# Kernel optimization log

Measured on AMD Instinct MI355X. Metric: run time of the kernel, lower is better.

## Reference

```python
import jax, jax.numpy as jnp
import numpy as np

BETA_MIN = 0.01
BETA_MAX = 0.995
EPS = 1e-6


def setup_inputs() -> dict:
    key = jax.random.key(0)
    k1, k2, k3, k4 = jax.random.split(key, 4)
    B, T, D = 16, 4096, 128
    return {
        "q": jax.random.normal(k1, (B, T, D), dtype=jnp.float32),
        "k": jax.random.normal(k2, (B, T, D), dtype=jnp.float32),
        "v": jax.random.normal(k3, (B, T, D), dtype=jnp.float32),
        "beta": jax.random.uniform(k4, (B, T, 1), dtype=jnp.float32),
        "mask": jnp.ones((B, T, 1), dtype=jnp.float32),
        "base_beta_1": jnp.asarray(2.0, dtype=jnp.float32),
        "base_beta_2": jnp.asarray(3.0, dtype=jnp.float32),
    }


def _delta_scan(q, k, v, beta, mask, base_beta_1, base_beta_2):
    B, T, D = q.shape
    phi_q = jax.nn.elu(q) + 1.0  # positive feature map
    phi_k = jax.nn.elu(k) + 1.0
    b1_base = jnp.clip(jax.nn.sigmoid(base_beta_1), BETA_MIN, BETA_MAX)
    b2_base = jnp.clip(jax.nn.sigmoid(base_beta_2), BETA_MIN, BETA_MAX)

    # time-major for scan: [T, B, ...]
    xs = (
        jnp.swapaxes(phi_q, 0, 1),
        jnp.swapaxes(phi_k, 0, 1),
        jnp.swapaxes(v, 0, 1),
        jnp.swapaxes(beta, 0, 1),
        jnp.swapaxes(mask, 0, 1),
    )

    H1 = jnp.zeros((B, D, D), dtype=q.dtype)
    H2 = jnp.zeros((B, D, D), dtype=q.dtype)
    Z1 = jnp.zeros((B, D), dtype=q.dtype)
    Z2 = jnp.zeros((B, D), dtype=q.dtype)

    def step(carry, x):
        H1, H2, Z1, Z2 = carry
        q_t, k_t, v_t, b_in_t, m_t = x  # q_t:[B,D], b_in_t/m_t:[B,1]
        b_in_t = jnp.clip(b_in_t, BETA_MIN, BETA_MAX)
        b1_t = jnp.clip(b1_base * b_in_t, BETA_MIN, BETA_MAX)  # [B,1]
        b2_t = jnp.clip(b2_base * b_in_t, BETA_MIN, BETA_MAX)
        kv = jnp.einsum('bd,be->bde', k_t, v_t) * m_t[:, :, None]  # masked outer product
        H1 = H1 * b1_t[:, :, None] + kv
        H2 = H2 * b2_t[:, :, None] + kv
        Z1 = Z1 * b1_t + k_t * m_t
        Z2 = Z2 * b2_t + k_t * m_t
        num = jnp.einsum('bd,bde->be', q_t, H1 + H2)
        den = jnp.maximum(jnp.sum(q_t * (Z1 + Z2), axis=-1, keepdims=True), EPS)
        o_t = num / den * m_t
        return (H1, H2, Z1, Z2), o_t

    _, outs = jax.lax.scan(step, (H1, H2, Z1, Z2), xs)
    return jnp.swapaxes(outs, 0, 1)  # [B, T, D]


def reference(q, k, v, beta, mask, base_beta_1, base_beta_2):
    return _delta_scan(q, k, v, beta, mask, base_beta_1, base_beta_2)
```

## Files before the change

### kernel.cpp

```cpp
#include <hip/hip_runtime.h>

#define B_ 16
#define T_ 4096
#define D_ 128
#define L_ 128
#define NC_ 32
#define CH_ (B_*NC_)
#define LDP 136

typedef __attribute__((ext_vector_type(8))) short bf16x8;
typedef __attribute__((ext_vector_type(4))) float f32x4;

__device__ __forceinline__ float clampf(float x, float lo, float hi) {
    return fminf(fmaxf(x, lo), hi);
}
__device__ __forceinline__ float phi_f(float x) {
    return x > 0.f ? x + 1.f : __expf(x);
}
__device__ __forceinline__ unsigned short bf16r(float f) {
    unsigned u = __builtin_bit_cast(unsigned, f);
    u += 0x7FFFu + ((u >> 16) & 1u);
    return (unsigned short)(u >> 16);
}
__device__ __forceinline__ float fbf(unsigned short h) {
    unsigned u = ((unsigned)h) << 16; return __builtin_bit_cast(float, u);
}
__device__ __forceinline__ unsigned pack2bf(float a, float b) {
    return (unsigned)bf16r(a) | ((unsigned)bf16r(b) << 16);
}
__device__ __forceinline__ uint4 pack8(const float* f) {
    uint4 r;
    r.x = pack2bf(f[0], f[1]); r.y = pack2bf(f[2], f[3]);
    r.z = pack2bf(f[4], f[5]); r.w = pack2bf(f[6], f[7]);
    return r;
}
__device__ __forceinline__ f32x4 zero4() { f32x4 z; z[0]=0.f; z[1]=0.f; z[2]=0.f; z[3]=0.f; return z; }

__device__ __forceinline__ int aidx(int row, int k0) {
    return (((row >> 4) * 4 + (k0 >> 5)) * 64 + ((k0 >> 3) & 3) * 16 + (row & 15)) * 8;
}

__global__ __launch_bounds__(256) void kS(
        const float* __restrict__ kk, const float* __restrict__ vv,
        const float* __restrict__ mask,
        const float* __restrict__ beta,
        const float* __restrict__ bb1, const float* __restrict__ bb2,
        unsigned short* __restrict__ phiKT, unsigned short* __restrict__ VtT,
        float* __restrict__ lg1, float* __restrict__ lg2, float* __restrict__ wexp) {
    int g = blockIdx.x;
    int ch = g >> 2, q = g & 3;
    int b = ch / NC_, c = ch % NC_;
    int tbase = b * T_ + c * L_;
    int tid = threadIdx.x;
    size_t cb = (size_t)ch * 16384;
    __shared__ float tot1s[2], tot2s[2];

    float cx1 = 0.f, cx2 = 0.f;
    int clane = tid & 63, cw = tid >> 6;
    if (q == 0 && tid < 128) {
        float b1b = clampf(1.f / (1.f + __expf(-bb1[0])), 0.01f, 0.995f);
        float b2b = clampf(1.f / (1.f + __expf(-bb2[0])), 0.01f, 0.995f);
        float be = clampf(beta[tbase + tid], 0.01f, 0.995f);
        cx1 = __logf(clampf(b1b * be, 0.01f, 0.995f));
        cx2 = __logf(clampf(b2b * be, 0.01f, 0.995f));
#pragma unroll
        for (int off = 1; off < 64; off <<= 1) {
            float y1 = __shfl_up(cx1, off);
            float y2 = __shfl_up(cx2, off);
            if (clane >= off) { cx1 += y1; cx2 += y2; }
        }
        if (clane == 63) { tot1s[cw] = cx1; tot2s[cw] = cx2; }
    }
    __syncthreads();
    if (q == 0 && tid < 128) {
        if (cw == 1) { cx1 += tot1s[0]; cx2 += tot2s[0]; }
        float tot1 = tot1s[0] + tot1s[1];
        float tot2 = tot2s[0] + tot2s[1];
        lg1[tbase + tid] = cx1;
        lg2[tbase + tid] = cx2;
        wexp[(size_t)ch * 128 + tid]                     = __expf(tot1 - cx1);
        wexp[(size_t)CH_ * 128 + (size_t)ch * 128 + tid] = __expf(tot2 - cx2);
    }

#pragma unroll
    for (int p = 0; p < 2; ++p) {
        int i = p * 256 + tid;
        int s = q * 32 + (i >> 4), d0 = (i & 15) * 8;
        const float* kp = &kk[(size_t)(tbase + s) * D_ + d0];
        float4 x0 = *(const float4*)kp, x1 = *(const float4*)(kp + 4);
        float m = mask[tbase + s];
        float pq[8] = {phi_f(x0.x)*m, phi_f(x0.y)*m, phi_f(x0.z)*m, phi_f(x0.w)*m,
                       phi_f(x1.x)*m, phi_f(x1.y)*m, phi_f(x1.z)*m, phi_f(x1.w)*m};
        *(uint4*)&phiKT[cb + aidx(s, d0)] = pack8(pq);
    }

#pragma unroll
    for (int p = 0; p < 2; ++p) {
        int i = p * 256 + tid;
        int e = q * 32 + (i & 31), s0 = (i >> 5) * 8;
        const float* vp = &vv[(size_t)(tbase + s0) * D_ + e];
        float f[8];
#pragma unroll
        for (int j = 0; j < 8; ++j)
            f[j] = vp[(size_t)j * D_];
        *(uint4*)&VtT[cb + aidx(e, s0)] = pack8(f);
    }
}

__global__ __launch_bounds__(512, 4) void kC(
        const unsigned short* __restrict__ phiKT,
        const unsigned short* __restrict__ VtT, const float* __restrict__ wexp,
        unsigned short* __restrict__ Cws, float* __restrict__ zc) {
    int g = blockIdx.x;
    int ch = ((g >> 4) << 3) | (g & 7);
    int st = (g >> 3) & 1;
    int b = ch / NC_, c = ch % NC_;
    int tid = threadIdx.x, lane = tid & 63, w = tid >> 6;
    int l15 = lane & 15, lg4 = lane >> 4;
    size_t cb = (size_t)ch * 16384;
    __shared__ unsigned short sKt[16384];

#pragma unroll
    for (int p = 0; p < 4; ++p) {
        int o = p * 512 + tid;
        uint4 pk = *(const uint4*)&phiKT[cb + (size_t)o * 8];
        int l15s = o & 15, kgrp = (o >> 4) & 3, ktile = (o >> 6) & 3, stile = o >> 8;
        int s = stile * 16 + l15s, d0 = ktile * 32 + kgrp * 8;
        unsigned short pu[8] = {
            (unsigned short)(pk.x & 0xffff), (unsigned short)(pk.x >> 16),
            (unsigned short)(pk.y & 0xffff), (unsigned short)(pk.y >> 16),
            (unsigned short)(pk.z & 0xffff), (unsigned short)(pk.z >> 16),
            (unsigned short)(pk.w & 0xffff), (unsigned short)(pk.w >> 16)};
#pragma unroll
        for (int j = 0; j < 8; ++j)
            sKt[aidx(d0 + j, s & ~7) + (s & 7)] = pu[j];
    }
    __syncthreads();

    const float* wp = &wexp[(size_t)st * CH_ * 128 + (size_t)ch * 128];

    f32x4 acc[8];
#pragma unroll
    for (int n = 0; n < 8; ++n) acc[n] = zero4();
    float zp[8] = {0.f, 0.f, 0.f, 0.f, 0.f, 0.f, 0.f, 0.f};

#pragma unroll
    for (int ks = 0; ks < 4; ++ks) {
        int koff = ks * 32 + lg4 * 8;
        float wl[8];
        {
            float4 a0 = *(const float4*)&wp[koff];
            float4 a1 = *(const float4*)&wp[koff + 4];
            wl[0]=a0.x; wl[1]=a0.y; wl[2]=a0.z; wl[3]=a0.w;
            wl[4]=a1.x; wl[5]=a1.y; wl[6]=a1.z; wl[7]=a1.w;
        }
        bf16x8 as;
        {
            bf16x8 vt = *(const bf16x8*)&VtT[cb + (size_t)(((w * 4 + ks) * 64 + lane) * 8)];
#pragma unroll
            for (int j = 0; j < 8; ++j)
                as[j] = (short)bf16r(fbf((unsigned short)vt[j]) * wl[j]);
        }
        bf16x8 bb[8];
#pragma unroll
        for (int n = 0; n < 8; ++n)
            bb[n] = *(const bf16x8*)&sKt[((n * 4 + ks) * 64 + lane) * 8];
        if (w == 0) {
#pragma unroll
            for (int n = 0; n < 8; ++n)
#pragma unroll
                for (int j = 0; j < 8; ++j)
                    zp[n] += wl[j] * fbf((unsigned short)bb[n][j]);
        }
#pragma unroll
        for (int n = 0; n < 8; ++n)
            acc[n] = __builtin_amdgcn_mfma_f32_16x16x32_bf16(as, bb[n], acc[n], 0, 0, 0);
    }

    if (w == 0) {
#pragma unroll
        for (int n = 0; n < 8; ++n) {
            float z = zp[n];
            z += __shfl_xor(z, 16); z += __shfl_xor(z, 32);
            if (lg4 == 0)
                zc[((size_t)(st * B_ + b) * NC_ + c) * D_ + n * 16 + l15] = z;
        }
    }

    __syncthreads();
#pragma unroll
    for (int n = 0; n < 8; ++n)
#pragma unroll
        for (int r = 0; r < 4; ++r) {
            int e = w * 16 + lg4 * 4 + r;
            int d = n * 16 + l15;
            sKt[aidx(e, d & ~7) + (d & 7)] = bf16r(acc[n][r]);
        }
    __syncthreads();
    unsigned short* Cp = Cws + ((size_t)(st * B_ + b) * NC_ + c) * (D_ * D_);
#pragma unroll
    for (int p = 0; p < 4; ++p) {
        int i = p * 512 + tid;
        *(uint4*)&Cp[(size_t)i * 8] = *(const uint4*)&sKt[i * 8];
    }
}

__global__ void k2f(unsigned short* __restrict__ Cws, float* __restrict__ zc,
                    const float* __restrict__ lg1, const float* __restrict__ lg2) {
    int g = blockIdx.x * blockDim.x + threadIdx.x;
    if (g < 131072) {
        int st = g >> 16;
        int rem = g & 65535;
        int b = rem >> 12;
        int de = (rem & 4095) * 4;
        const float* lg = st ? lg2 : lg1;
        size_t base = ((size_t)(st * B_ + b) * NC_) * (D_ * D_) + de;
        float run0 = 0.f, run1 = 0.f, run2 = 0.f, run3 = 0.f;
#pragma unroll
        for (int c = 0; c < NC_; c++) {
            float a = __expf(lg[b * T_ + c * L_ + L_ - 1]);
            uint2 val = *(uint2*)&Cws[base + (size_t)c * (D_ * D_)];
            float t0 = fbf((unsigned short)(val.x & 0xffff)), t1 = fbf((unsigned short)(val.x >> 16));
            float t2 = fbf((unsigned short)(val.y & 0xffff)), t3 = fbf((unsigned short)(val.y >> 16));
            uint2 wv; wv.x = pack2bf(run0, run1); wv.y = pack2bf(run2, run3);
            *(uint2*)&Cws[base + (size_t)c * (D_ * D_)] = wv;
            run0 = a * run0 + t0; run1 = a * run1 + t1;
            run2 = a * run2 + t2; run3 = a * run3 + t3;
        }
    } else {
        int gz = g - 131072;
        int st = gz >> 11;
        int rem = gz & 2047;
        int b = rem >> 7;
        int d = rem & 127;
        const float* lg = st ? lg2 : lg1;
        size_t base = ((size_t)(st * B_ + b) * NC_) * D_ + d;
        float run = 0.f;
#pragma unroll
        for (int c = 0; c < NC_; c++) {
            float a = __expf(lg[b * T_ + c * L_ + L_ - 1]);
            float tmp = zc[base + (size_t)c * D_];
            zc[base + (size_t)c * D_] = run;
            run = a * run + tmp;
        }
    }
}

__global__ __launch_bounds__(512, 2) void k3_v13(
        const float* __restrict__ qq, const float* __restrict__ mask,
        const float* __restrict__ lg1, const float* __restrict__ lg2,
        const unsigned short* __restrict__ phiKT, const unsigned short* __restrict__ VtT,
        const unsigned short* __restrict__ Cws, const float* __restrict__ zc,
        float* __restrict__ out) {
    __shared__ unsigned short sQ[128 * LDP];
    __shared__ unsigned short bufP[8][16 * LDP];
    __shared__ float sOsc[128], sA1[128], sA2[128];
    int ch = blockIdx.x;
    int b = ch / NC_, c = ch % NC_;
    int tbase = b * T_ + c * L_;
    int tid = threadIdx.x, lane = tid & 63, w = tid >> 6;
    int l15 = lane & 15, lg4 = lane >> 4;
    size_t cb = (size_t)ch * 16384;
    unsigned short* sPK = &bufP[0][0];

#pragma unroll
    for (int p = 0; p < 4; ++p) {
        int i = p * 512 + tid;
        *(uint4*)&sPK[i * 8] = *(const uint4*)&phiKT[cb + (size_t)i * 8];
    }
#pragma unroll
    for (int p = 0; p < 8; ++p) {
        int i = p * 512 + tid;
        int t = i >> 5, d4 = (i & 31) * 4;
        float4 x = *(const float4*)&qq[(size_t)(tbase + t) * D_ + d4];
        uint2 dd;
        dd.x = pack2bf(phi_f(x.x), phi_f(x.y));
        dd.y = pack2bf(phi_f(x.z), phi_f(x.w));
        *(uint2*)&sQ[t * LDP + d4] = dd;
    }

    int trow = w * 16 + l15;
    size_t gt = (size_t)(tbase + trow);
    float lg1t = lg1[gt], lg2t = lg2[gt], mt = mask[gt];
    float a1t = __expf(lg1t), a2t = __expf(lg2t);

    __syncthreads();

    bf16x8 qf[4];
#pragma unroll
    for (int ks = 0; ks < 4; ++ks)
        qf[ks] = *(const bf16x8*)&sQ[trow * LDP + ks * 32 + lg4 * 8];

    const float* z1p = &zc[((size_t)(0 * B_ + b) * NC_ + c) * D_];
    const float* z2p = &zc[((size_t)(1 * B_ + b) * NC_ + c) * D_];
    float d1 = 0.f, d2 = 0.f;
#pragma unroll
    for (int ks = 0; ks < 4; ++ks) {
        int off = ks * 32 + lg4 * 8;
        float4 za = *(const float4*)(z1p + off), zb = *(const float4*)(z1p + off + 4);
        float4 zca = *(const float4*)(z2p + off), zcb = *(const float4*)(z2p + off + 4);
        float z1a[8] = {za.x, za.y, za.z, za.w, zb.x, zb.y, zb.z, zb.w};
        float z2a[8] = {zca.x, zca.y, zca.z, zca.w, zcb.x, zcb.y, zcb.z, zcb.w};
#pragma unroll
        for (int j = 0; j < 8; ++j) {
            float fq = fbf((unsigned short)qf[ks][j]);
            d1 += fq * z1a[j]; d2 += fq * z2a[j];
        }
    }
    d1 += __shfl_xor(d1, 16); d1 += __shfl_xor(d1, 32);
    d2 += __shfl_xor(d2, 16); d2 += __shfl_xor(d2, 32);

    int SN = (w | 1) + 1;
    int KP = SN >> 1;
    f32x4 accs[8];
#pragma unroll
    for (int x = 0; x < 8; ++x) accs[x] = zero4();
#pragma unroll
    for (int sp = 0; sp < 4; ++sp) {
        if (sp < KP) {
            bf16x8 kf[8];
#pragma unroll
            for (int mm = 0; mm < 2; ++mm)
#pragma unroll
                for (int ks = 0; ks < 4; ++ks)
                    kf[mm * 4 + ks] = *(const bf16x8*)&sPK[((((sp * 2 + mm) * 4) + ks) * 64 + lane) * 8];
#pragma unroll
            for (int ks = 0; ks < 4; ++ks) {
                accs[sp * 2 + 0] = __builtin_amdgcn_mfma_f32_16x16x32_bf16(kf[ks],     qf[ks], accs[sp * 2 + 0], 0, 0, 0);
                accs[sp * 2 + 1] = __builtin_amdgcn_mfma_f32_16x16x32_bf16(kf[4 + ks], qf[ks], accs[sp * 2 + 1], 0, 0, 0);
            }
        }
    }
    __syncthreads();

    float rs = 0.f;
#pragma unroll
    for (int sp = 0; sp < 4; ++sp) {
        if (sp < KP) {
#pragma unroll
            for (int mm = 0; mm < 2; ++mm) {
                int s0 = (sp * 2 + mm) * 16 + lg4 * 4;
                float4 l1s = *(const float4*)&lg1[tbase + s0];
                float4 l2s = *(const float4*)&lg2[tbase + s0];
                float l1a[4] = {l1s.x, l1s.y, l1s.z, l1s.w};
                float l2a[4] = {l2s.x, l2s.y, l2s.z, l2s.w};
                float pv[4];
#pragma unroll
                for (int r = 0; r < 4; ++r) {
                    int s = s0 + r;
                    float p = 0.f;
                    if (s <= trow)
                        p = accs[sp * 2 + mm][r] * (__expf(lg1t - l1a[r]) + __expf(lg2t - l2a[r]));
                    pv[r] = p; rs += p;
                }
                uint2 dd; dd.x = pack2bf(pv[0], pv[1]); dd.y = pack2bf(pv[2], pv[3]);
                *(uint2*)&bufP[w][l15 * LDP + s0] = dd;
            }
        }
    }
    rs += __shfl_xor(rs, 16); rs += __shfl_xor(rs, 32);
    float osc = mt / fmaxf(a1t * d1 + a2t * d2 + rs, 1e-6f);
    if (lg4 == 0) {
        sOsc[trow] = osc;
        sA1[trow] = a1t;
        sA2[trow] = a2t;
    }
    __syncthreads();

    {
        int m = w;
        bf16x8 vf[4];
#pragma unroll
        for (int ks = 0; ks < 4; ++ks)
            vf[ks] = *(const bf16x8*)&VtT[cb + (size_t)(((m * 4 + ks) * 64 + lane) * 8)];

        f32x4 accO[8];
#pragma unroll
        for (int tt = 0; tt < 8; ++tt) accO[tt] = zero4();

#pragma unroll
        for (int st = 0; st < 2; ++st) {
            const unsigned short* Hp = Cws + ((size_t)(st * B_ + b) * NC_ + c) * (D_ * D_);
            bf16x8 hf[4];
#pragma unroll
            for (int ks = 0; ks < 4; ++ks)
                hf[ks] = *(const bf16x8*)&Hp[(size_t)(((m * 4 + ks) * 64 + lane) * 8)];
            f32x4 U[8];
#pragma unroll
            for (int tt = 0; tt < 8; ++tt) U[tt] = zero4();
#pragma unroll
            for (int ks = 0; ks < 4; ++ks) {
                int koff = ks * 32 + lg4 * 8;
#pragma unroll
                for (int tt = 0; tt < 8; ++tt) {
                    bf16x8 qb = *(const bf16x8*)&sQ[(tt * 16 + l15) * LDP + koff];
                    U[tt] = __builtin_amdgcn_mfma_f32_16x16x32_bf16(hf[ks], qb, U[tt], 0, 0, 0);
                }
            }
            const float* sA = st ? sA2 : sA1;
#pragma unroll
            for (int tt = 0; tt < 8; ++tt) {
                float sc = sA[tt * 16 + l15];
#pragma unroll
                for (int r = 0; r < 4; ++r) accO[tt][r] += sc * U[tt][r];
            }
        }

#pragma unroll
        for (int tt = 0; tt < 8; ++tt) {
            int KPt = ((tt | 1) + 1) >> 1;
            for (int ks = 0; ks < KPt; ++ks) {
                bf16x8 pf = *(const bf16x8*)&bufP[tt][l15 * LDP + ks * 32 + lg4 * 8];
                accO[tt] = __builtin_amdgcn_mfma_f32_16x16x32_bf16(vf[ks], pf, accO[tt], 0, 0, 0);
            }
        }

#pragma unroll
        for (int tt = 0; tt < 8; ++tt) {
            float oscr = sOsc[tt * 16 + l15];
            f32x4 o;
            o[0] = accO[tt][0] * oscr; o[1] = accO[tt][1] * oscr;
            o[2] = accO[tt][2] * oscr; o[3] = accO[tt][3] * oscr;
            f32x4* op = (f32x4*)&out[(size_t)(tbase + tt * 16 + l15) * D_ + m * 16 + lg4 * 4];
            __builtin_nontemporal_store(o, op);
        }
    }
}

extern "C" void kernel_launch(void* const* d_in, const int* in_sizes, int n_in,
                              void* d_out, int out_size, void* d_ws, size_t ws_size,
                              hipStream_t stream) {
    const float* q    = (const float*)d_in[0];
    const float* k    = (const float*)d_in[1];
    const float* v    = (const float*)d_in[2];
    const float* beta = (const float*)d_in[3];
    const float* mask = (const float*)d_in[4];
    const float* bb1  = (const float*)d_in[5];
    const float* bb2  = (const float*)d_in[6];
    float* out = (float*)d_out;

    size_t n_lg = (size_t)B_ * T_;
    size_t n_z  = (size_t)2 * B_ * NC_ * D_;
    size_t n_w  = (size_t)2 * CH_ * 128;
    size_t n_C  = (size_t)2 * B_ * NC_ * D_ * D_;
    size_t n_kt = (size_t)B_ * T_ * D_;
    size_t need = (2 * n_lg + n_z + n_w) * sizeof(float) + (n_C + 2 * n_kt) * sizeof(unsigned short);
    if (ws_size < need) return;

    float* lg1  = (float*)d_ws;
    float* lg2  = lg1 + n_lg;
    float* zc   = lg2 + n_lg;
    float* wexp = zc + n_z;
    unsigned short* Cws    = (unsigned short*)(wexp + n_w);
    unsigned short* phiKT  = Cws + n_C;
    unsigned short* VtT    = phiKT + n_kt;

    kS<<<4 * CH_, 256, 0, stream>>>(k, v, mask, beta, bb1, bb2, phiKT, VtT, lg1, lg2, wexp);
    kC<<<2 * CH_, 512, 0, stream>>>(phiKT, VtT, wexp, Cws, zc);
    k2f<<<528, 256, 0, stream>>>(Cws, zc, lg1, lg2);
    k3_v13<<<CH_, 512, 0, stream>>>(q, mask, lg1, lg2, phiKT, VtT, Cws, zc, out);
}
```

Before: 76.09 us.

## Fuse chunk staging and chunk-state MFMA kernels into one 1024-thread kernel

Merges the kS staging kernel and the kC chunk-state kernel into a single kernel with one 1024-thread block per chunk. Transposed phi(K) and V are built directly in shared memory, and the decay weights stay in LDS, so the wexp global buffer and the global round trip of K/V into kC go away. Sixteen waves now compute both decay streams together. In exchange the grid is smaller with larger blocks, k is read twice from global in different layouts, and the 64KB of LDS per block may limit occupancy.

```diff
diff --git a/kernel.cpp b/kernel.cpp
--- a/kernel.cpp
+++ b/kernel.cpp
@@ -40,24 +40,29 @@
     return (((row >> 4) * 4 + (k0 >> 5)) * 64 + ((k0 >> 3) & 3) * 16 + (row & 15)) * 8;
 }
 
-__global__ __launch_bounds__(256) void kS(
+__global__ __launch_bounds__(1024, 4) void kSC(
+        const float* __restrict__ beta,
+        const float* __restrict__ bb1, const float* __restrict__ bb2,
         const float* __restrict__ kk, const float* __restrict__ vv,
         const float* __restrict__ mask,
-        const float* __restrict__ beta,
-        const float* __restrict__ bb1, const float* __restrict__ bb2,
+        float* __restrict__ lg1, float* __restrict__ lg2,
         unsigned short* __restrict__ phiKT, unsigned short* __restrict__ VtT,
-        float* __restrict__ lg1, float* __restrict__ lg2, float* __restrict__ wexp) {
-    int g = blockIdx.x;
-    int ch = g >> 2, q = g & 3;
+        unsigned short* __restrict__ Cws, float* __restrict__ zc) {
+    int ch = blockIdx.x;
     int b = ch / NC_, c = ch % NC_;
     int tbase = b * T_ + c * L_;
-    int tid = threadIdx.x;
+    int tid = threadIdx.x, lane = tid & 63, w = tid >> 6;
+    int l15 = lane & 15, lg4 = lane >> 4;
     size_t cb = (size_t)ch * 16384;
+
+    __shared__ unsigned short sKt[16384];
+    __shared__ unsigned short sVt[16384];
+    __shared__ float wL[2][128];
     __shared__ float tot1s[2], tot2s[2];
 
     float cx1 = 0.f, cx2 = 0.f;
-    int clane = tid & 63, cw = tid >> 6;
-    if (q == 0 && tid < 128) {
+    if (tid < 128) {
+        int cl = tid & 63, cw = tid >> 6;
         float b1b = clampf(1.f / (1.f + __expf(-bb1[0])), 0.01f, 0.995f);
         float b2b = clampf(1.f / (1.f + __expf(-bb2[0])), 0.01f, 0.995f);
         float be = clampf(beta[tbase + tid], 0.01f, 0.995f);
@@ -67,25 +72,48 @@
         for (int off = 1; off < 64; off <<= 1) {
             float y1 = __shfl_up(cx1, off);
             float y2 = __shfl_up(cx2, off);
-            if (clane >= off) { cx1 += y1; cx2 += y2; }
-        }
-        if (clane == 63) { tot1s[cw] = cx1; tot2s[cw] = cx2; }
-    }
-    __syncthreads();
-    if (q == 0 && tid < 128) {
-        if (cw == 1) { cx1 += tot1s[0]; cx2 += tot2s[0]; }
+            if (cl >= off) { cx1 += y1; cx2 += y2; }
+        }
+        if (cl == 63) { tot1s[cw] = cx1; tot2s[cw] = cx2; }
+    }
+    __syncthreads();
+    if (tid < 128) {
+        if (tid >= 64) { cx1 += tot1s[0]; cx2 += tot2s[0]; }
         float tot1 = tot1s[0] + tot1s[1];
         float tot2 = tot2s[0] + tot2s[1];
         lg1[tbase + tid] = cx1;
         lg2[tbase + tid] = cx2;
-        wexp[(size_t)ch * 128 + tid]                     = __expf(tot1 - cx1);
-        wexp[(size_t)CH_ * 128 + (size_t)ch * 128 + tid] = __expf(tot2 - cx2);
+        wL[0][tid] = __expf(tot1 - cx1);
+        wL[1][tid] = __expf(tot2 - cx2);
     }
 
 #pragma unroll
     for (int p = 0; p < 2; ++p) {
-        int i = p * 256 + tid;
-        int s = q * 32 + (i >> 4), d0 = (i & 15) * 8;
+        int i = p * 1024 + tid;
+        int d = i & 127, s0 = (i >> 7) * 8;
+        const float* kp = &kk[(size_t)(tbase + s0) * D_ + d];
+        const float* mp = &mask[tbase + s0];
+        float f[8];
+#pragma unroll
+        for (int j = 0; j < 8; ++j)
+            f[j] = phi_f(kp[(size_t)j * D_]) * mp[j];
+        *(uint4*)&sKt[aidx(d, s0)] = pack8(f);
+    }
+#pragma unroll
+    for (int p = 0; p < 2; ++p) {
+        int i = p * 1024 + tid;
+        int e = i & 127, s0 = (i >> 7) * 8;
+        const float* vp = &vv[(size_t)(tbase + s0) * D_ + e];
+        float f[8];
+#pragma unroll
+        for (int j = 0; j < 8; ++j)
+            f[j] = vp[(size_t)j * D_];
+        *(uint4*)&sVt[aidx(e, s0)] = pack8(f);
+    }
+#pragma unroll
+    for (int p = 0; p < 2; ++p) {
+        int i = p * 1024 + tid;
+        int s = i >> 4, d0 = (i & 15) * 8;
         const float* kp = &kk[(size_t)(tbase + s) * D_ + d0];
         float4 x0 = *(const float4*)kp, x1 = *(const float4*)(kp + 4);
         float m = mask[tbase + s];
@@ -93,52 +121,16 @@
                        phi_f(x1.x)*m, phi_f(x1.y)*m, phi_f(x1.z)*m, phi_f(x1.w)*m};
         *(uint4*)&phiKT[cb + aidx(s, d0)] = pack8(pq);
     }
+    __syncthreads();
 
 #pragma unroll
     for (int p = 0; p < 2; ++p) {
-        int i = p * 256 + tid;
-        int e = q * 32 + (i & 31), s0 = (i >> 5) * 8;
-        const float* vp = &vv[(size_t)(tbase + s0) * D_ + e];
-        float f[8];
-#pragma unroll
-        for (int j = 0; j < 8; ++j)
-            f[j] = vp[(size_t)j * D_];
-        *(uint4*)&VtT[cb + aidx(e, s0)] = pack8(f);
-    }
-}
-
-__global__ __launch_bounds__(512, 4) void kC(
-        const unsigned short* __restrict__ phiKT,
-        const unsigned short* __restrict__ VtT, const float* __restrict__ wexp,
-        unsigned short* __restrict__ Cws, float* __restrict__ zc) {
-    int g = blockIdx.x;
-    int ch = ((g >> 4) << 3) | (g & 7);
-    int st = (g >> 3) & 1;
-    int b = ch / NC_, c = ch % NC_;
-    int tid = threadIdx.x, lane = tid & 63, w = tid >> 6;
-    int l15 = lane & 15, lg4 = lane >> 4;
-    size_t cb = (size_t)ch * 16384;
-    __shared__ unsigned short sKt[16384];
-
-#pragma unroll
-    for (int p = 0; p < 4; ++p) {
-        int o = p * 512 + tid;
-        uint4 pk = *(const uint4*)&phiKT[cb + (size_t)o * 8];
-        int l15s = o & 15, kgrp = (o >> 4) & 3, ktile = (o >> 6) & 3, stile = o >> 8;
-        int s = stile * 16 + l15s, d0 = ktile * 32 + kgrp * 8;
-        unsigned short pu[8] = {
-            (unsigned short)(pk.x & 0xffff), (unsigned short)(pk.x >> 16),
-            (unsigned short)(pk.y & 0xffff), (unsigned short)(pk.y >> 16),
-            (unsigned short)(pk.z & 0xffff), (unsigned short)(pk.z >> 16),
-            (unsigned short)(pk.w & 0xffff), (unsigned short)(pk.w >> 16)};
-#pragma unroll
-        for (int j = 0; j < 8; ++j)
-            sKt[aidx(d0 + j, s & ~7) + (s & 7)] = pu[j];
-    }
-    __syncthreads();
-
-    const float* wp = &wexp[(size_t)st * CH_ * 128 + (size_t)ch * 128];
-
+        int o = p * 1024 + tid;
+        *(uint4*)&VtT[cb + (size_t)o * 8] = *(const uint4*)&sVt[o * 8];
+    }
+
+    int st = w >> 3, m = w & 7;
+    const float* wp = &wL[st][0];
     f32x4 acc[8];
 #pragma unroll
     for (int n = 0; n < 8; ++n) acc[n] = zero4();
@@ -148,15 +140,11 @@
     for (int ks = 0; ks < 4; ++ks) {
         int koff = ks * 32 + lg4 * 8;
         float wl[8];
-        {
-            float4 a0 = *(const float4*)&wp[koff];
-            float4 a1 = *(const float4*)&wp[koff + 4];
-            wl[0]=a0.x; wl[1]=a0.y; wl[2]=a0.z; wl[3]=a0.w;
-            wl[4]=a1.x; wl[5]=a1.y; wl[6]=a1.z; wl[7]=a1.w;
-        }
+#pragma unroll
+        for (int j = 0; j < 8; ++j) wl[j] = wp[koff + j];
         bf16x8 as;
         {
-            bf16x8 vt = *(const bf16x8*)&VtT[cb + (size_t)(((w * 4 + ks) * 64 + lane) * 8)];
+            bf16x8 vt = *(const bf16x8*)&sVt[((m * 4 + ks) * 64 + lane) * 8];
 #pragma unroll
             for (int j = 0; j < 8; ++j)
                 as[j] = (short)bf16r(fbf((unsigned short)vt[j]) * wl[j]);
@@ -165,7 +153,7 @@
 #pragma unroll
         for (int n = 0; n < 8; ++n)
             bb[n] = *(const bf16x8*)&sKt[((n * 4 + ks) * 64 + lane) * 8];
-        if (w == 0) {
+        if (m == 0) {
 #pragma unroll
             for (int n = 0; n < 8; ++n)
 #pragma unroll
@@ -177,7 +165,7 @@
             acc[n] = __builtin_amdgcn_mfma_f32_16x16x32_bf16(as, bb[n], acc[n], 0, 0, 0);
     }
 
-    if (w == 0) {
+    if (m == 0) {
 #pragma unroll
         for (int n = 0; n < 8; ++n) {
             float z = zp[n];
@@ -188,20 +176,25 @@
     }
 
     __syncthreads();
-#pragma unroll
-    for (int n = 0; n < 8; ++n)
-#pragma unroll
-        for (int r = 0; r < 4; ++r) {
-            int e = w * 16 + lg4 * 4 + r;
-            int d = n * 16 + l15;
-            sKt[aidx(e, d & ~7) + (d & 7)] = bf16r(acc[n][r]);
-        }
-    __syncthreads();
-    unsigned short* Cp = Cws + ((size_t)(st * B_ + b) * NC_ + c) * (D_ * D_);
-#pragma unroll
-    for (int p = 0; p < 4; ++p) {
-        int i = p * 512 + tid;
-        *(uint4*)&Cp[(size_t)i * 8] = *(const uint4*)&sKt[i * 8];
+    {
+        unsigned short* dst = st ? sVt : sKt;
+#pragma unroll
+        for (int n = 0; n < 8; ++n)
+#pragma unroll
+            for (int r = 0; r < 4; ++r) {
+                int e = m * 16 + lg4 * 4 + r;
+                int d = n * 16 + l15;
+                dst[aidx(e, d & ~7) + (d & 7)] = bf16r(acc[n][r]);
+            }
+    }
+    __syncthreads();
+    unsigned short* Cp0 = Cws + ((size_t)(0 * B_ + b) * NC_ + c) * (D_ * D_);
+    unsigned short* Cp1 = Cws + ((size_t)(1 * B_ + b) * NC_ + c) * (D_ * D_);
+#pragma unroll
+    for (int p = 0; p < 2; ++p) {
+        int o = p * 1024 + tid;
+        *(uint4*)&Cp0[(size_t)o * 8] = *(const uint4*)&sKt[o * 8];
+        *(uint4*)&Cp1[(size_t)o * 8] = *(const uint4*)&sVt[o * 8];
     }
 }
 
@@ -441,22 +434,19 @@
 
     size_t n_lg = (size_t)B_ * T_;
     size_t n_z  = (size_t)2 * B_ * NC_ * D_;
-    size_t n_w  = (size_t)2 * CH_ * 128;
     size_t n_C  = (size_t)2 * B_ * NC_ * D_ * D_;
     size_t n_kt = (size_t)B_ * T_ * D_;
-    size_t need = (2 * n_lg + n_z + n_w) * sizeof(float) + (n_C + 2 * n_kt) * sizeof(unsigned short);
+    size_t need = (2 * n_lg + n_z) * sizeof(float) + (n_C + 2 * n_kt) * sizeof(unsigned short);
     if (ws_size < need) return;
 
     float* lg1  = (float*)d_ws;
     float* lg2  = lg1 + n_lg;
     float* zc   = lg2 + n_lg;
-    float* wexp = zc + n_z;
-    unsigned short* Cws    = (unsigned short*)(wexp + n_w);
+    unsigned short* Cws    = (unsigned short*)(zc + n_z);
     unsigned short* phiKT  = Cws + n_C;
     unsigned short* VtT    = phiKT + n_kt;
 
-    kS<<<4 * CH_, 256, 0, stream>>>(k, v, mask, beta, bb1, bb2, phiKT, VtT, lg1, lg2, wexp);
-    kC<<<2 * CH_, 512, 0, stream>>>(phiKT, VtT, wexp, Cws, zc);
+    kSC<<<CH_, 1024, 0, stream>>>(beta, bb1, bb2, k, v, mask, lg1, lg2, phiKT, VtT, Cws, zc);
     k2f<<<528, 256, 0, stream>>>(Cws, zc, lg1, lg2);
     k3_v13<<<CH_, 512, 0, stream>>>(q, mask, lg1, lg2, phiKT, VtT, Cws, zc, out);
 }
```

Result: no change. 75.33 us, median of 2 (-1.0%).
